# Performance work log

Measured on AMD Instinct MI355X. Metric: run time of the kernel, lower is better.

The kernel has to match this reference:

```python
import jax, jax.numpy as jnp
import numpy as np

B, I, H = 16384, 512, 512


def setup_inputs() -> dict:
    key = jax.random.key(0)
    ks = jax.random.split(key, 10)
    inputs = jax.random.normal(ks[0], (B, I), dtype=jnp.float32)
    state = jax.random.normal(ks[1], (B, 2 * H), dtype=jnp.float32)
    # xavier_uniform for w_ih: U(-a, a), a = sqrt(6 / (fan_in + fan_out))
    a = float(np.sqrt(6.0 / (2 * H + I)))
    w_ih = jax.random.uniform(ks[2], (2 * H, I), jnp.float32, -a, a)
    b_h = jnp.zeros((H,), jnp.float32)
    pi = float(np.pi)
    d1 = jax.random.uniform(ks[3], (H,), jnp.float32, -pi, pi)
    d2 = jax.random.uniform(ks[4], (H,), jnp.float32, -pi, pi)
    d3 = jax.random.uniform(ks[5], (H,), jnp.float32, -pi, pi)
    re1 = jax.random.uniform(ks[6], (H,), jnp.float32, -1.0, 1.0)
    im1 = jax.random.uniform(ks[7], (H,), jnp.float32, -1.0, 1.0)
    re2 = jax.random.uniform(ks[8], (H,), jnp.float32, -1.0, 1.0)
    im2 = jax.random.uniform(ks[9], (H,), jnp.float32, -1.0, 1.0)
    perm = jnp.asarray(np.random.default_rng(0).permutation(H), dtype=jnp.int32)
    return {"inputs": inputs, "state": state, "w_ih": w_ih, "b_h": b_h,
            "d1": d1, "d2": d2, "d3": d3,
            "re1": re1, "im1": im1, "re2": re2, "im2": im2, "perm": perm}


def _diag_mul(w, z):
    # multiply by exp(i*w) built as complex(cos w, sin w), as in the original
    return jax.lax.complex(jnp.cos(w), jnp.sin(w)) * z


def _reflect(re, im, z):
    # z - (2/||v||^2) * (z @ conj(v)) outer v   (faithful to original matmuls)
    v = jax.lax.complex(re, im)                 # [H]
    vz = z @ jnp.conj(v)                        # [B]
    factor = 2.0 / jnp.sum(re * re + im * im)   # real scalar
    return z - factor * vz[:, None] * v[None, :]


def _modrelu(z, b):
    norm = jnp.abs(z)
    scale = jax.nn.relu(norm + b) / (norm + 1e-6)
    return z * scale


def reference(inputs, state, w_ih, b_h, d1, d2, d3, re1, im1, re2, im2, perm):
    inputs_mul = inputs @ w_ih.T                                  # [B, 2H]
    z_in = jax.lax.complex(inputs_mul[:, :H], inputs_mul[:, H:])  # [B, H] c64
    state_c = jax.lax.complex(state[:, :H], state[:, H:])
    # Unitary chain (computed in original forward, but its result `preact` is
    # never used for the returned state -- faithfully reproduced).
    s = _diag_mul(d1, state_c)
    s = jnp.fft.fft(s, axis=-1)
    s = _reflect(re1, im1, s)
    s = s[:, perm]                 # column permutation (z.T[P].T)
    s = _diag_mul(d2, s)
    s = jnp.fft.ifft(s, axis=-1)
    s = _reflect(re2, im2, s)
    s = _diag_mul(d3, s)
    preact = z_in + s              # dead in original; kept for fidelity
    new_state_c = _modrelu(z_in, b_h)
    return jnp.concatenate([jnp.real(new_state_c), jnp.imag(new_state_c)], axis=1)
```

## Files before the change

### kernel.cpp

```cpp
#include <hip/hip_runtime.h>
#include <hip/hip_bf16.h>


typedef __attribute__((ext_vector_type(8))) short bf16x8;
typedef __attribute__((ext_vector_type(4))) float f32x4;

#define BM 256
#define BK 64
#define KDIM 512
#define NDIM 1024
#define NKT (KDIM / BK)

__device__ __forceinline__ unsigned short f2bf(float f) {
    unsigned u = __builtin_bit_cast(unsigned, f);
    u += 0x7fffu + ((u >> 16) & 1u);
    return (unsigned short)(u >> 16);
}

__global__ __launch_bounds__(256) void cvt_w(const float* __restrict__ W,
                                             unsigned short* __restrict__ Wbf, int n4) {
    int i = blockIdx.x * blockDim.x + threadIdx.x;
    int stride = gridDim.x * blockDim.x;
    for (; i < n4; i += stride) {
        float4 v = reinterpret_cast<const float4*>(W)[i];
        ushort4 o;
        o.x = f2bf(v.x); o.y = f2bf(v.y); o.z = f2bf(v.z); o.w = f2bf(v.w);
        reinterpret_cast<ushort4*>(Wbf)[i] = o;
    }
}

__device__ __forceinline__ void gload_lds16(const void* g, void* l) {
    __builtin_amdgcn_global_load_lds(
        (const __attribute__((address_space(1))) unsigned int*)g,
        (__attribute__((address_space(3))) unsigned int*)l, 16, 0, 0);
}

__global__ __launch_bounds__(512, 2) void gemm_modrelu(
    const float* __restrict__ A,
    const unsigned short* __restrict__ W,
    const float* __restrict__ bh,
    float* __restrict__ out)
{
    __shared__ unsigned short At[2][BM * BK];
    __shared__ unsigned short Bt[2][BM * BK];

    const int tid = threadIdx.x;
    const int w   = tid >> 6;
    const int l   = tid & 63;
    const int l15 = l & 15;
    const int l4  = l >> 4;
    const int wm  = w >> 2;
    const int wn  = w & 3;

    const int bx = blockIdx.x;
    const int lg = (bx & 7) * 32 + (bx >> 3);
    const int mb = lg >> 2;
    const int cb = lg & 3;

    const int arow0 = tid >> 4;
    const int aseg  = tid & 15;
    const int aswz  = (arow0 & 7) << 3;
    const float4* ga[8];
#pragma unroll
    for (int s = 0; s < 8; ++s)
        ga[s] = reinterpret_cast<const float4*>(
                    A + (size_t)(mb * BM + s * 32 + arow0) * KDIM) + aseg;

    const int srow = l >> 3;
    const int sseg = (l & 7) ^ srow;
    const unsigned short* gb[4];
    int ldso[4];
#pragma unroll
    for (int is = 0; is < 4; ++is) {
        int row  = w * 32 + is * 8 + srow;
        int wrow = (row >> 7) * 512 + cb * 128 + (row & 127);
        gb[is]   = W + (size_t)wrow * KDIM + sseg * 8;
        ldso[is] = (w * 32 + is * 8) * BK;
    }

    float4 ra[8];
    auto load_a = [&](int kt) {
#pragma unroll
        for (int s = 0; s < 8; ++s) ra[s] = ga[s][kt * (BK / 4)];
    };
    auto write_a = [&](int buf) {
#pragma unroll
        for (int s = 0; s < 8; ++s) {
            ushort4 o;
            o.x = f2bf(ra[s].x); o.y = f2bf(ra[s].y);
            o.z = f2bf(ra[s].z); o.w = f2bf(ra[s].w);
            int row = s * 32 + arow0;
            *reinterpret_cast<ushort4*>(&At[buf][row * BK + ((aseg * 4) ^ aswz)]) = o;
        }
    };
    auto stage_b = [&](int kt, int buf) {
#pragma unroll
        for (int is = 0; is < 4; ++is)
            gload_lds16(gb[is] + kt * BK, &Bt[buf][ldso[is]]);
    };

    f32x4 acc[8][4];
#pragma unroll
    for (int i = 0; i < 8; ++i)
#pragma unroll
        for (int j = 0; j < 4; ++j) acc[i][j] = f32x4{0.f, 0.f, 0.f, 0.f};

    load_a(0);
    asm volatile("s_waitcnt vmcnt(0)" ::: "memory");
    write_a(0);
    stage_b(0, 0);
    load_a(1);
    stage_b(1, 1);
    asm volatile("s_waitcnt vmcnt(12) lgkmcnt(0)" ::: "memory");
    __builtin_amdgcn_s_barrier();

#pragma unroll
    for (int kt = 0; kt < NKT; ++kt) {
        const int buf = kt & 1;

        if (kt + 1 < NKT) {
            asm volatile("s_waitcnt vmcnt(4)" ::: "memory");
            write_a(buf ^ 1);
        }
        if (kt + 2 < NKT) load_a(kt + 2);

#pragma unroll
        for (int ks = 0; ks < 2; ++ks) {
            bf16x8 af[8], bf[4];
            const int slot = (ks * 4 + l4);
#pragma unroll
            for (int i = 0; i < 8; ++i) {
                int row = wm * 128 + i * 16 + l15;
                af[i] = *(const bf16x8*)(&At[buf][row * BK + (slot ^ (row & 7)) * 8]);
            }
#pragma unroll
            for (int jn = 0; jn < 4; ++jn) {
                int row = (jn < 2) ? (wn * 32 + jn * 16 + l15)
                                   : (128 + wn * 32 + (jn - 2) * 16 + l15);
                bf[jn] = *(const bf16x8*)(&Bt[buf][row * BK + (slot ^ (row & 7)) * 8]);
            }
            asm volatile("s_waitcnt lgkmcnt(0)" ::: "memory");
            __builtin_amdgcn_sched_barrier(0);
            __builtin_amdgcn_s_setprio(1);
#pragma unroll
            for (int i = 0; i < 8; ++i)
#pragma unroll
                for (int jn = 0; jn < 4; ++jn)
                    acc[i][jn] = __builtin_amdgcn_mfma_f32_16x16x32_bf16(
                        af[i], bf[jn], acc[i][jn], 0, 0, 0);
            __builtin_amdgcn_s_setprio(0);
        }

        if (kt + 1 < NKT) {
            __builtin_amdgcn_s_barrier();
            if (kt + 2 < NKT) asm volatile("s_waitcnt vmcnt(8)" ::: "memory");
            else              asm volatile("s_waitcnt vmcnt(0)" ::: "memory");
            if (kt + 2 < NKT) stage_b(kt + 2, buf);
            __builtin_amdgcn_s_barrier();
        }
    }

#pragma unroll
    for (int jn = 0; jn < 2; ++jn) {
        int n = cb * 128 + wn * 32 + jn * 16 + l15;
        float b = bh[n];
#pragma unroll
        for (int i = 0; i < 8; ++i) {
#pragma unroll
            for (int j = 0; j < 4; ++j) {
                int m = mb * BM + wm * 128 + i * 16 + l4 * 4 + j;
                float re  = acc[i][jn][j];
                float imv = acc[i][jn + 2][j];
                float norm  = sqrtf(re * re + imv * imv);
                float scale = fmaxf(norm + b, 0.f) * __builtin_amdgcn_rcpf(norm + 1e-6f);
                float* po = out + (size_t)m * NDIM + n;
                __builtin_nontemporal_store(re  * scale, po);
                __builtin_nontemporal_store(imv * scale, po + 512);
            }
        }
    }
}

extern "C" void kernel_launch(void* const* d_in, const int* in_sizes, int n_in,
                              void* d_out, int out_size, void* d_ws, size_t ws_size,
                              hipStream_t stream) {
    const float* inputs = (const float*)d_in[0];
    const float* w_ih   = (const float*)d_in[2];
    const float* b_h    = (const float*)d_in[3];
    float* out = (float*)d_out;

    unsigned short* Wbf = (unsigned short*)d_ws;

    cvt_w<<<512, 256, 0, stream>>>(w_ih, Wbf, (1024 * 512) / 4);

    gemm_modrelu<<<256, 512, 0, stream>>>(inputs, Wbf, b_h, out);
}
```

Before: 47.55 us.

## Shrink GEMM tiles to 128x128, deepen A prefetch, interleave LDS reads with MFMA

The fused GEMM+modReLU kernel now uses 128-row by 128-column tiles (64 complex columns) with 256 threads and launches 1024 blocks instead of 256, which gives more parallelism across CUs. The A operand gets a three-deep register prefetch. The fp32-to-bf16 conversion now uses the packed v_cvt_pk_bf16_f32 instruction. LDS fragment reads for the second k-half are split so they overlap with the A writes and MFMAs of the first half. Smaller tiles lower the arithmetic intensity per block and add more reloads of A and W from L2, and the extra prefetch registers raise register pressure.

```diff
diff --git a/kernel.cpp b/kernel.cpp
--- a/kernel.cpp
+++ b/kernel.cpp
@@ -5,11 +5,14 @@
 typedef __attribute__((ext_vector_type(8))) short bf16x8;
 typedef __attribute__((ext_vector_type(4))) float f32x4;
 
-#define BM 256
+#define BM 128
 #define BK 64
 #define KDIM 512
 #define NDIM 1024
-#define NKT (KDIM / BK)
+#define NKT 8
+
+#define VMCNT(n) asm volatile("s_waitcnt vmcnt(" #n ")" ::: "memory")
+#define LGKM(n)  asm volatile("s_waitcnt lgkmcnt(" #n ")" ::: "memory")
 
 __device__ __forceinline__ unsigned short f2bf(float f) {
     unsigned u = __builtin_bit_cast(unsigned, f);
@@ -35,7 +38,13 @@
         (__attribute__((address_space(3))) unsigned int*)l, 16, 0, 0);
 }
 
-__global__ __launch_bounds__(512, 2) void gemm_modrelu(
+__device__ __forceinline__ unsigned cvtpk(float lo, float hi) {
+    unsigned r;
+    asm("v_cvt_pk_bf16_f32 %0, %1, %2" : "=v"(r) : "v"(lo), "v"(hi));
+    return r;
+}
+
+__global__ __launch_bounds__(256, 2) void gemm_modrelu(
     const float* __restrict__ A,
     const unsigned short* __restrict__ W,
     const float* __restrict__ bh,
@@ -49,22 +58,19 @@
     const int l   = tid & 63;
     const int l15 = l & 15;
     const int l4  = l >> 4;
-    const int wm  = w >> 2;
-    const int wn  = w & 3;
+    const int wm  = w >> 1;
+    const int wn  = w & 1;
 
     const int bx = blockIdx.x;
-    const int lg = (bx & 7) * 32 + (bx >> 3);
-    const int mb = lg >> 2;
-    const int cb = lg & 3;
+    const int lg = (bx & 7) * 128 + (bx >> 3);
+    const int mb = lg >> 3;
+    const int cb = lg & 7;
 
     const int arow0 = tid >> 4;
     const int aseg  = tid & 15;
     const int aswz  = (arow0 & 7) << 3;
-    const float4* ga[8];
-#pragma unroll
-    for (int s = 0; s < 8; ++s)
-        ga[s] = reinterpret_cast<const float4*>(
-                    A + (size_t)(mb * BM + s * 32 + arow0) * KDIM) + aseg;
+    const float4* gA = reinterpret_cast<const float4*>(A) + (size_t)(mb * BM) * (KDIM / 4);
+    const int abase = arow0 * (KDIM / 4) + aseg;
 
     const int srow = l >> 3;
     const int sseg = (l & 7) ^ srow;
@@ -73,24 +79,25 @@
 #pragma unroll
     for (int is = 0; is < 4; ++is) {
         int row  = w * 32 + is * 8 + srow;
-        int wrow = (row >> 7) * 512 + cb * 128 + (row & 127);
+        int wrow = (row >> 6) * 512 + cb * 64 + (row & 63);
         gb[is]   = W + (size_t)wrow * KDIM + sseg * 8;
         ldso[is] = (w * 32 + is * 8) * BK;
     }
 
-    float4 ra[8];
-    auto load_a = [&](int kt) {
-#pragma unroll
-        for (int s = 0; s < 8; ++s) ra[s] = ga[s][kt * (BK / 4)];
+    float4 ra[3][8];
+    auto load_a = [&](int kt, int set) {
+#pragma unroll
+        for (int s = 0; s < 8; ++s)
+            ra[set][s] = gA[(size_t)s * 16 * (KDIM / 4) + abase + kt * (BK / 4)];
     };
-    auto write_a = [&](int buf) {
+    auto write_a = [&](int buf, int set) {
 #pragma unroll
         for (int s = 0; s < 8; ++s) {
-            ushort4 o;
-            o.x = f2bf(ra[s].x); o.y = f2bf(ra[s].y);
-            o.z = f2bf(ra[s].z); o.w = f2bf(ra[s].w);
-            int row = s * 32 + arow0;
-            *reinterpret_cast<ushort4*>(&At[buf][row * BK + ((aseg * 4) ^ aswz)]) = o;
+            uint2 o;
+            o.x = cvtpk(ra[set][s].x, ra[set][s].y);
+            o.y = cvtpk(ra[set][s].z, ra[set][s].w);
+            int row = s * 16 + arow0;
+            *reinterpret_cast<uint2*>(&At[buf][row * BK + ((aseg * 4) ^ aswz)]) = o;
         }
     };
     auto stage_b = [&](int kt, int buf) {
@@ -99,62 +106,76 @@
             gload_lds16(gb[is] + kt * BK, &Bt[buf][ldso[is]]);
     };
 
-    f32x4 acc[8][4];
-#pragma unroll
-    for (int i = 0; i < 8; ++i)
+    f32x4 acc[4][4];
+#pragma unroll
+    for (int i = 0; i < 4; ++i)
 #pragma unroll
         for (int j = 0; j < 4; ++j) acc[i][j] = f32x4{0.f, 0.f, 0.f, 0.f};
 
-    load_a(0);
-    asm volatile("s_waitcnt vmcnt(0)" ::: "memory");
-    write_a(0);
+    load_a(0, 0);
+    load_a(1, 1);
     stage_b(0, 0);
-    load_a(1);
+    load_a(2, 2);
     stage_b(1, 1);
-    asm volatile("s_waitcnt vmcnt(12) lgkmcnt(0)" ::: "memory");
+    VMCNT(24);
+    write_a(0, 0);
+    VMCNT(12);
+    LGKM(0);
     __builtin_amdgcn_s_barrier();
 
 #pragma unroll
     for (int kt = 0; kt < NKT; ++kt) {
         const int buf = kt & 1;
 
-        if (kt + 1 < NKT) {
-            asm volatile("s_waitcnt vmcnt(4)" ::: "memory");
-            write_a(buf ^ 1);
-        }
-        if (kt + 2 < NKT) load_a(kt + 2);
-
-#pragma unroll
-        for (int ks = 0; ks < 2; ++ks) {
-            bf16x8 af[8], bf[4];
-            const int slot = (ks * 4 + l4);
-#pragma unroll
-            for (int i = 0; i < 8; ++i) {
-                int row = wm * 128 + i * 16 + l15;
-                af[i] = *(const bf16x8*)(&At[buf][row * BK + (slot ^ (row & 7)) * 8]);
-            }
-#pragma unroll
-            for (int jn = 0; jn < 4; ++jn) {
-                int row = (jn < 2) ? (wn * 32 + jn * 16 + l15)
-                                   : (128 + wn * 32 + (jn - 2) * 16 + l15);
-                bf[jn] = *(const bf16x8*)(&Bt[buf][row * BK + (slot ^ (row & 7)) * 8]);
-            }
-            asm volatile("s_waitcnt lgkmcnt(0)" ::: "memory");
-            __builtin_amdgcn_sched_barrier(0);
-            __builtin_amdgcn_s_setprio(1);
-#pragma unroll
-            for (int i = 0; i < 8; ++i)
-#pragma unroll
-                for (int jn = 0; jn < 4; ++jn)
-                    acc[i][jn] = __builtin_amdgcn_mfma_f32_16x16x32_bf16(
-                        af[i], bf[jn], acc[i][jn], 0, 0, 0);
-            __builtin_amdgcn_s_setprio(0);
-        }
+        bf16x8 af[4], bf[4];
+#pragma unroll
+        for (int i = 0; i < 4; ++i) {
+            int row = wm * 64 + i * 16 + l15;
+            af[i] = *(const bf16x8*)(&At[buf][row * BK + (l4 ^ (row & 7)) * 8]);
+        }
+#pragma unroll
+        for (int j = 0; j < 4; ++j) {
+            int row = (j >> 1) * 64 + wn * 32 + (j & 1) * 16 + l15;
+            bf[j] = *(const bf16x8*)(&Bt[buf][row * BK + (l4 ^ (row & 7)) * 8]);
+        }
+        if (kt + 1 < NKT) write_a(buf ^ 1, (kt + 1) % 3);
+        if (kt + 3 < NKT) load_a(kt + 3, (kt + 3) % 3);
+
+        if (kt + 1 < NKT) { LGKM(8); } else { LGKM(0); }
+        __builtin_amdgcn_sched_barrier(0);
+        __builtin_amdgcn_s_setprio(1);
+#pragma unroll
+        for (int i = 0; i < 4; ++i)
+#pragma unroll
+            for (int j = 0; j < 4; ++j)
+                acc[i][j] = __builtin_amdgcn_mfma_f32_16x16x32_bf16(
+                    af[i], bf[j], acc[i][j], 0, 0, 0);
+        __builtin_amdgcn_s_setprio(0);
+
+#pragma unroll
+        for (int i = 0; i < 4; ++i) {
+            int row = wm * 64 + i * 16 + l15;
+            af[i] = *(const bf16x8*)(&At[buf][row * BK + ((4 + l4) ^ (row & 7)) * 8]);
+        }
+#pragma unroll
+        for (int j = 0; j < 4; ++j) {
+            int row = (j >> 1) * 64 + wn * 32 + (j & 1) * 16 + l15;
+            bf[j] = *(const bf16x8*)(&Bt[buf][row * BK + ((4 + l4) ^ (row & 7)) * 8]);
+        }
+        LGKM(0);
+        __builtin_amdgcn_sched_barrier(0);
+        __builtin_amdgcn_s_setprio(1);
+#pragma unroll
+        for (int i = 0; i < 4; ++i)
+#pragma unroll
+            for (int j = 0; j < 4; ++j)
+                acc[i][j] = __builtin_amdgcn_mfma_f32_16x16x32_bf16(
+                    af[i], bf[j], acc[i][j], 0, 0, 0);
+        __builtin_amdgcn_s_setprio(0);
 
         if (kt + 1 < NKT) {
             __builtin_amdgcn_s_barrier();
-            if (kt + 2 < NKT) asm volatile("s_waitcnt vmcnt(8)" ::: "memory");
-            else              asm volatile("s_waitcnt vmcnt(0)" ::: "memory");
+            if (kt <= 4) { VMCNT(8); } else { VMCNT(0); }
             if (kt + 2 < NKT) stage_b(kt + 2, buf);
             __builtin_amdgcn_s_barrier();
         }
@@ -162,13 +183,13 @@
 
 #pragma unroll
     for (int jn = 0; jn < 2; ++jn) {
-        int n = cb * 128 + wn * 32 + jn * 16 + l15;
+        int n = cb * 64 + wn * 32 + jn * 16 + l15;
         float b = bh[n];
 #pragma unroll
-        for (int i = 0; i < 8; ++i) {
+        for (int i = 0; i < 4; ++i) {
 #pragma unroll
             for (int j = 0; j < 4; ++j) {
-                int m = mb * BM + wm * 128 + i * 16 + l4 * 4 + j;
+                int m = mb * BM + wm * 64 + i * 16 + l4 * 4 + j;
                 float re  = acc[i][jn][j];
                 float imv = acc[i][jn + 2][j];
                 float norm  = sqrtf(re * re + imv * imv);
@@ -191,7 +212,7 @@
 
     unsigned short* Wbf = (unsigned short*)d_ws;
 
-    cvt_w<<<512, 256, 0, stream>>>(w_ih, Wbf, (1024 * 512) / 4);
-
-    gemm_modrelu<<<256, 512, 0, stream>>>(inputs, Wbf, b_h, out);
-}
+    cvt_w<<<256, 256, 0, stream>>>(w_ih, Wbf, (1024 * 512) / 4);
+
+    gemm_modrelu<<<1024, 256, 0, stream>>>(inputs, Wbf, b_h, out);
+}
```

New measurement: 41.57 us. 12.6% less time.
